# Kernel tuning notes

Measured on AMD Instinct MI355X. Metric: run time of the kernel, lower is better.

Reference implementation:

```python
import jax, jax.numpy as jnp
import numpy as np

B, S, D_MODEL, D_FF, N_EXPERTS, TOP_K = 4, 1024, 1024, 4096, 24, 2


def setup_inputs() -> dict:
    key = jax.random.key(0)
    ks = jax.random.split(key, 7)
    sd = 1.0 / np.sqrt(D_MODEL)
    sf = 1.0 / np.sqrt(D_FF)
    return {
        "x": jax.random.normal(ks[0], (B, S, D_MODEL), jnp.float32),
        "gate_w": jax.random.uniform(ks[1], (D_MODEL, N_EXPERTS), jnp.float32, -sd, sd),
        "gate_b": jax.random.uniform(ks[2], (N_EXPERTS,), jnp.float32, -sd, sd),
        "w1": jax.random.uniform(ks[3], (N_EXPERTS, D_MODEL, D_FF), jnp.float32, -sd, sd),
        "b1": jax.random.uniform(ks[4], (N_EXPERTS, D_FF), jnp.float32, -sd, sd),
        "w2": jax.random.uniform(ks[5], (N_EXPERTS, D_FF, D_MODEL), jnp.float32, -sf, sf),
        "b2": jax.random.uniform(ks[6], (N_EXPERTS, D_MODEL), jnp.float32, -sf, sf),
    }


def reference(x, gate_w, gate_b, w1, b1, w2, b2):
    b, s, d = x.shape
    xt = x.reshape(-1, d)                      # [T, d_model]
    t = xt.shape[0]
    scores = xt @ gate_w + gate_b              # [T, E]
    topv, topi = jax.lax.top_k(scores, TOP_K)  # [T, k]
    gates = jax.nn.softmax(topv, axis=-1)      # softmax over the top-k logits
    # combine weights per (token, expert); zero for unselected experts
    cw = jnp.zeros((t, N_EXPERTS), x.dtype).at[jnp.arange(t)[:, None], topi].add(gates)
    out = jnp.zeros_like(xt)
    for e in range(N_EXPERTS):
        h = jax.nn.gelu(xt @ w1[e] + b1[e], approximate=False)
        y = h @ w2[e] + b2[e]
        out = out + cw[:, e:e + 1] * y
    return out.reshape(b, s, d)
```

## Files before the change

### kernel.cpp

```cpp
#include <hip/hip_runtime.h>
#include <hip/hip_bf16.h>
#include <math.h>

#define T_TOKENS 4096
#define DMODEL 1024
#define DFF 4096
#define NEXP 24
#define NSLOTS 8192
#define BKP 40

typedef __attribute__((ext_vector_type(8))) short bf16x8;
typedef __attribute__((ext_vector_type(4))) float f32x4;
typedef __attribute__((ext_vector_type(8))) unsigned short us8;

static __device__ __forceinline__ unsigned short f2bf(float f) {
    union { float f; unsigned u; } v; v.f = f;
    unsigned r = v.u + 0x7fffu + ((v.u >> 16) & 1u);
    return (unsigned short)(r >> 16);
}

__global__ void k_zero(int* __restrict__ p) { p[threadIdx.x] = 0; }

__global__ __launch_bounds__(256) void k_gate(
    const float* __restrict__ x, const float* __restrict__ gw,
    const float* __restrict__ gb, int* __restrict__ topk_e,
    float* __restrict__ topk_g, int* __restrict__ counts)
{
    __shared__ float xs[8][1024];
    __shared__ float sc[8][24];
    __shared__ int lcnt[24];
    int tid = threadIdx.x;
    int t0 = blockIdx.x * 8;
    #pragma unroll
    for (int i = 0; i < 8; i++) {
        int idx = tid + 256*i;
        int r = idx >> 8, c4 = (idx & 255) * 4;
        *(float4*)&xs[r][c4] = *(const float4*)(x + (size_t)(t0+r)*DMODEL + c4);
    }
    if (tid < 24) lcnt[tid] = 0;
    __syncthreads();

    int tok = tid >> 5, e = tid & 31;
    if (e < NEXP) {
        float s0=0.f, s1=0.f, s2=0.f, s3=0.f;
        #pragma unroll 4
        for (int d = 0; d < DMODEL; d += 4) {
            s0 += xs[tok][d]   * gw[(d  )*NEXP + e];
            s1 += xs[tok][d+1] * gw[(d+1)*NEXP + e];
            s2 += xs[tok][d+2] * gw[(d+2)*NEXP + e];
            s3 += xs[tok][d+3] * gw[(d+3)*NEXP + e];
        }
        sc[tok][e] = (s0+s1)+(s2+s3) + gb[e];
    }
    __syncthreads();

    if (tid < 8) {
        int t = t0 + tid;
        float v0=-1e30f, v1=-1e30f; int i0=0, i1=0;
        #pragma unroll
        for (int ee = 0; ee < NEXP; ee++) {
            float s = sc[tid][ee];
            if (s > v0) { v1=v0; i1=i0; v0=s; i0=ee; }
            else if (s > v1) { v1=s; i1=ee; }
        }
        float e1 = expf(v1 - v0);
        float g0 = 1.f/(1.f+e1), g1 = e1/(1.f+e1);
        topk_e[t*2]=i0; topk_e[t*2+1]=i1;
        topk_g[t*2]=g0; topk_g[t*2+1]=g1;
        atomicAdd(&lcnt[i0], 1); atomicAdd(&lcnt[i1], 1);
    }
    __syncthreads();
    if (tid < NEXP && lcnt[tid]) atomicAdd(&counts[tid], lcnt[tid]);
}

__global__ void k_scan(const int* __restrict__ counts, int* __restrict__ offsets) {
    if (threadIdx.x == 0) {
        int run = 0;
        for (int e = 0; e < NEXP; e++) { offsets[e] = run; run += counts[e]; }
        offsets[NEXP] = run;
    }
}

__global__ __launch_bounds__(256) void k_assign(
    const int* __restrict__ topk_e, const float* __restrict__ topk_g,
    const int* __restrict__ offsets, int* __restrict__ counts2,
    int* __restrict__ slot_token, float* __restrict__ slot_gate,
    int* __restrict__ slot_of)
{
    int idx = blockIdx.x * 256 + threadIdx.x;
    if (idx >= NSLOTS) return;
    int e = topk_e[idx];
    int pos = offsets[e] + atomicAdd(&counts2[e], 1);
    slot_token[pos] = idx >> 1;
    slot_gate[pos] = topk_g[idx];
    slot_of[idx] = pos;
}

__global__ __launch_bounds__(256) void k_xgather(
    const float* __restrict__ x, const int* __restrict__ slot_token,
    unsigned short* __restrict__ xg)
{
    int idx = blockIdx.x * 256 + threadIdx.x;
    int slot = idx >> 7, c8 = (idx & 127) * 8;
    int tok = slot_token[slot];
    const float4* p = (const float4*)(x + (size_t)tok * DMODEL + c8);
    float4 v0 = p[0], v1 = p[1];
    us8 o;
    o[0]=f2bf(v0.x); o[1]=f2bf(v0.y); o[2]=f2bf(v0.z); o[3]=f2bf(v0.w);
    o[4]=f2bf(v1.x); o[5]=f2bf(v1.y); o[6]=f2bf(v1.z); o[7]=f2bf(v1.w);
    *(us8*)(xg + (size_t)slot * DMODEL + c8) = o;
}


#define FFN_BODY(LDA, LDB, NTT)                                                \
    int tid = threadIdx.x, l = tid & 63, wv = tid >> 6;                        \
    int wm = (wv >> 1) * 48, wn = (wv & 1) * 64;                               \
    int lrow = l & 15, lkg = l >> 4;                                           \
    f32x4 acc[3][4];                                                           \
    _Pragma("unroll")                                                          \
    for (int i = 0; i < 3; i++)                                                \
      _Pragma("unroll")                                                        \
      for (int j = 0; j < 4; j++)                                              \
        acc[i][j] = (f32x4){0.f, 0.f, 0.f, 0.f};                               \
    int n4 = (tid & 31) * 4;                                                   \
    int dwk = tid >> 5;                          \
    int arow0 = tid >> 2, ac0 = tid & 3;                                       \
    int arow1 = 128 + (tid >> 2);                                              \
    int apc0 = ac0 ^ ((arow0 >> 1) & 3);                                       \
    int apc1 = ac0 ^ ((arow1 >> 1) & 3);                                       \
    int mBw = (tid & 31) & 7;                  \
    int pdw = 2 * ((dwk >> 1) ^ mBw) + (dwk & 1);                              \
    float4 br0, br1; us8 ar0, ar1;                                             \
    auto issue = [&](int t) {                                                  \
        int k0 = t * 32;                                                       \
        const float* p = wb + (size_t)(k0 + dwk*2) * LDB + n4;                 \
        br0 = *(const float4*)p;                                               \
        br1 = *(const float4*)(p + LDB);                                       \
        ar0 = *(const us8*)(ag + (size_t)arow0 * LDA + k0 + ac0 * 8);          \
        if (tid < 256)                                                         \
            ar1 = *(const us8*)(ag + (size_t)arow1 * LDA + k0 + ac0 * 8);      \
    };                                                                         \
    auto wr = [&]() {                                                          \
        _Pragma("unroll")                                                      \
        for (int j = 0; j < 4; j++) {                                          \
            int nn = n4 + j;                                                   \
            unsigned u;                                                        \
            asm("v_cvt_pk_bf16_f32 %0, %1, %2" : "=v"(u)                       \
                : "v"(((const float*)&br0)[j]), "v"(((const float*)&br1)[j])); \
            *(unsigned*)&Bs[nn*BKP + 2*pdw] = u;                               \
        }                                                                      \
        *(us8*)&As[arow0*32 + apc0*8] = ar0;                                   \
        if (tid < 256)                                                         \
            *(us8*)&As[arow1*32 + apc1*8] = ar1;                               \
    };                                                                         \
    issue(0);                                                                  \
    for (int t = 0; t < NTT; t++) {                                            \
        __syncthreads();                                                       \
        wr();                                                                  \
        if (t + 1 < NTT) issue(t + 1);                                         \
        __syncthreads();                                                       \
        bf16x8 a[3];                                                           \
        _Pragma("unroll")                                                      \
        for (int ms = 0; ms < 3; ms++) {                                       \
            int r = wm + ms*16 + lrow;                                         \
            int c = lkg ^ ((r >> 1) & 3);                                      \
            a[ms] = *(const bf16x8*)&As[r*32 + c*8];                           \
        }                                                                      \
        union BV { uint2 q[2]; bf16x8 v; } b[4];                               \
        _Pragma("unroll")                                                      \
        for (int ni = 0; ni < 4; ni++) {                                       \
            int nb = wn + ni*16 + lrow;                                        \
            int mB = (nb >> 2) & 7;                                            \
            b[ni].q[0] = *(const uint2*)&Bs[nb*BKP + 4*((2*lkg) ^ mB)];        \
            b[ni].q[1] = *(const uint2*)&Bs[nb*BKP + 4*((2*lkg + 1) ^ mB)];    \
        }                                                                      \
        _Pragma("unroll")                                                      \
        for (int ms = 0; ms < 3; ms++)                                         \
          _Pragma("unroll")                                                    \
          for (int ni = 0; ni < 4; ni++)                                       \
            acc[ms][ni] = __builtin_amdgcn_mfma_f32_16x16x32_bf16(             \
                a[ms], b[ni].v, acc[ms][ni], 0, 0, 0);                         \
    }

__global__ __launch_bounds__(512) void k_ffn1(
    const unsigned short* __restrict__ xg, const float* __restrict__ w1,
    const float* __restrict__ b1, const int* __restrict__ offsets,
    unsigned short* __restrict__ hbuf)
{
    int bid = blockIdx.x;
    int xcd = bid & 7, s = bid >> 3;
    int eg = s / 96, rem = s % 96;
    int nx = rem / 3, mt = rem % 3;
    int e = eg * 8 + xcd;

    int base = offsets[e], ne = offsets[e+1] - base;
    if (mt * 192 >= ne) return;
    int n0 = nx * 128;
    int slotbase = base + mt * 192;

    __shared__ unsigned short As[192*32];
    __shared__ unsigned short Bs[128*BKP];

    const unsigned short* ag = xg + (size_t)slotbase * DMODEL;
    const float* wb = w1 + (size_t)e * DMODEL * DFF + n0;

    FFN_BODY(DMODEL, DFF, (DMODEL/32))

    #pragma unroll
    for (int ms = 0; ms < 3; ms++) {
        #pragma unroll
        for (int ni = 0; ni < 4; ni++) {
            int n = n0 + wn + ni*16 + lrow;
            float bias = b1[e*DFF + n];
            #pragma unroll
            for (int r = 0; r < 4; r++) {
                int ml = wm + ms*16 + lkg*4 + r;
                if (mt*192 + ml < ne) {
                    float hv = acc[ms][ni][r] + bias;
                    hv = 0.5f * hv * (1.f + erff(hv * 0.70710678118f));
                    hbuf[(size_t)(slotbase + ml) * DFF + n] = f2bf(hv);
                }
            }
        }
    }
}

__global__ __launch_bounds__(512) void k_ffn2(
    const unsigned short* __restrict__ hbuf, const float* __restrict__ w2,
    const float* __restrict__ b2, const int* __restrict__ offsets,
    const float* __restrict__ slot_gate, float* __restrict__ y)
{
    int bid = blockIdx.x;
    int xcd = bid & 7, s = bid >> 3;
    int eg = s / 24, rem = s % 24;
    int nx = rem / 3, mt = rem % 3;
    int e = eg * 8 + xcd;

    int base = offsets[e], ne = offsets[e+1] - base;
    if (mt * 192 >= ne) return;
    int n0 = nx * 128;
    int slotbase = base + mt * 192;

    __shared__ unsigned short As[192*32];
    __shared__ unsigned short Bs[128*BKP];
    __shared__ float gat[192];

    if (threadIdx.x < 192)
        gat[threadIdx.x] = (mt*192 + threadIdx.x < ne) ? slot_gate[slotbase + threadIdx.x] : 0.f;

    const unsigned short* ag = hbuf + (size_t)slotbase * DFF;
    const float* wb = w2 + (size_t)e * DFF * DMODEL + n0;

    FFN_BODY(DFF, DMODEL, (DFF/32))

    #pragma unroll
    for (int ms = 0; ms < 3; ms++) {
        #pragma unroll
        for (int ni = 0; ni < 4; ni++) {
            int n = n0 + wn + ni*16 + lrow;
            float bias = b2[e*DMODEL + n];
            #pragma unroll
            for (int r = 0; r < 4; r++) {
                int ml = wm + ms*16 + lkg*4 + r;
                if (mt*192 + ml < ne) {
                    y[(size_t)(slotbase + ml) * DMODEL + n] = gat[ml] * (acc[ms][ni][r] + bias);
                }
            }
        }
    }
}

__global__ __launch_bounds__(256) void k_combine(
    const float* __restrict__ y, const int* __restrict__ slot_of,
    float* __restrict__ out)
{
    int t = blockIdx.x, tid = threadIdx.x;
    int s0 = slot_of[t*2], s1 = slot_of[t*2+1];
    float4 a = ((const float4*)(y + (size_t)s0 * DMODEL))[tid];
    float4 b = ((const float4*)(y + (size_t)s1 * DMODEL))[tid];
    float4 o = {a.x+b.x, a.y+b.y, a.z+b.z, a.w+b.w};
    ((float4*)(out + (size_t)t * DMODEL))[tid] = o;
}

extern "C" void kernel_launch(void* const* d_in, const int* in_sizes, int n_in,
                              void* d_out, int out_size, void* d_ws, size_t ws_size,
                              hipStream_t stream) {
    const float* x  = (const float*)d_in[0];
    const float* gw = (const float*)d_in[1];
    const float* gb = (const float*)d_in[2];
    const float* w1 = (const float*)d_in[3];
    const float* b1 = (const float*)d_in[4];
    const float* w2 = (const float*)d_in[5];
    const float* b2 = (const float*)d_in[6];
    float* out = (float*)d_out;
    char* ws = (char*)d_ws;

    int*   counts     = (int*)(ws + 0);
    int*   counts2    = (int*)(ws + 128);
    int*   offsets    = (int*)(ws + 256);
    int*   topk_e     = (int*)(ws + 512);
    float* topk_g     = (float*)(ws + 33280);
    int*   slot_token = (int*)(ws + 66048);
    float* slot_gate  = (float*)(ws + 99328);
    int*   slot_of    = (int*)(ws + 132608);
    unsigned short* xg = (unsigned short*)(ws + 1048576);
    float*          y  = (float*)(ws + 1048576);
    unsigned short* hbuf = (unsigned short*)(ws + 35651584);

    k_zero<<<1, 128, 0, stream>>>((int*)ws);

    k_gate<<<T_TOKENS/8, 256, 0, stream>>>(x, gw, gb, topk_e, topk_g, counts);
    k_scan<<<1, 64, 0, stream>>>(counts, offsets);
    k_assign<<<NSLOTS/256, 256, 0, stream>>>(topk_e, topk_g, offsets, counts2,
                                             slot_token, slot_gate, slot_of);
    k_xgather<<<NSLOTS*128/256, 256, 0, stream>>>(x, slot_token, xg);

    k_ffn1<<<dim3(8 * 288), 512, 0, stream>>>(xg, w1, b1, offsets, hbuf);

    k_ffn2<<<dim3(8 * 72), 512, 0, stream>>>(hbuf, w2, b2, offsets, slot_gate, y);

    k_combine<<<T_TOKENS, 256, 0, stream>>>(y, slot_of, out);
}
```

Measured before the change: 463.0 us.

## Double-buffer A via direct global-to-LDS loads and retile FFN GEMMs to 128x128

Rewrites the shared FFN GEMM body. The A operand is now copied straight from global memory into double-buffered LDS with global_load_lds, and explicit waitcnt/barrier scheduling lets the next tile's loads overlap the current compute. Blocks shrink from 512 threads with 192-row tiles to 256 threads with 128-row tiles, each wave computing 64x64. This aims to hide load latency and cut register staging, but adds launch-grid blocks and relies on hand-written vmcnt counts that must stay exact.

```diff
diff --git a/kernel.cpp b/kernel.cpp
--- a/kernel.cpp
+++ b/kernel.cpp
@@ -17,6 +17,12 @@
     union { float f; unsigned u; } v; v.f = f;
     unsigned r = v.u + 0x7fffu + ((v.u >> 16) & 1u);
     return (unsigned short)(r >> 16);
+}
+
+typedef const __attribute__((address_space(1))) void gvoid_t;
+typedef __attribute__((address_space(3))) void lvoid_t;
+static __device__ __forceinline__ void gl_lds16(const void* g, void* l) {
+    __builtin_amdgcn_global_load_lds((gvoid_t*)g, (lvoid_t*)l, 16, 0, 0);
 }
 
 __global__ void k_zero(int* __restrict__ p) { p[threadIdx.x] = 0; }
@@ -112,102 +118,123 @@
 }
 
 
-#define FFN_BODY(LDA, LDB, NTT)                                                \
+#define FFN_PIPE(LDA, LDB, NTT)                                                \
     int tid = threadIdx.x, l = tid & 63, wv = tid >> 6;                        \
-    int wm = (wv >> 1) * 48, wn = (wv & 1) * 64;                               \
+    int wm = (wv >> 1) * 64, wn = (wv & 1) * 64;                               \
     int lrow = l & 15, lkg = l >> 4;                                           \
-    f32x4 acc[3][4];                                                           \
+    f32x4 acc[4][4];                                                           \
     _Pragma("unroll")                                                          \
-    for (int i = 0; i < 3; i++)                                                \
+    for (int i = 0; i < 4; i++)                                                \
       _Pragma("unroll")                                                        \
       for (int j = 0; j < 4; j++)                                              \
         acc[i][j] = (f32x4){0.f, 0.f, 0.f, 0.f};                               \
-    int n4 = (tid & 31) * 4;                                                   \
-    int dwk = tid >> 5;                          \
-    int arow0 = tid >> 2, ac0 = tid & 3;                                       \
-    int arow1 = 128 + (tid >> 2);                                              \
-    int apc0 = ac0 ^ ((arow0 >> 1) & 3);                                       \
-    int apc1 = ac0 ^ ((arow1 >> 1) & 3);                                       \
-    int mBw = (tid & 31) & 7;                  \
-    int pdw = 2 * ((dwk >> 1) ^ mBw) + (dwk & 1);                              \
-    float4 br0, br1; us8 ar0, ar1;                                             \
-    auto issue = [&](int t) {                                                  \
-        int k0 = t * 32;                                                       \
-        const float* p = wb + (size_t)(k0 + dwk*2) * LDB + n4;                 \
-        br0 = *(const float4*)p;                                               \
-        br1 = *(const float4*)(p + LDB);                                       \
-        ar0 = *(const us8*)(ag + (size_t)arow0 * LDA + k0 + ac0 * 8);          \
-        if (tid < 256)                                                         \
-            ar1 = *(const us8*)(ag + (size_t)arow1 * LDA + k0 + ac0 * 8);      \
+    int n4 = (tid & 31) * 4, q7 = tid & 7, kq = (tid >> 5) * 4;                \
+    int cbw = (tid >> 5) ^ q7;                   \
+    int ar0 = tid >> 2;                                                        \
+    int as0 = (tid & 3) ^ ((ar0 >> 1) & 3);                                    \
+    int ar1 = 64 + ar0;                                                        \
+    int as1 = (tid & 3) ^ ((ar1 >> 1) & 3);                                    \
+    float4 br[4];                                                              \
+    auto issueB = [&](int t) {                                                 \
+        const float* pp = wb + (size_t)(t*32 + kq) * LDB + n4;                 \
+        br[0] = *(const float4*)pp;                                            \
+        br[1] = *(const float4*)(pp + LDB);                                    \
+        br[2] = *(const float4*)(pp + 2*LDB);                                  \
+        br[3] = *(const float4*)(pp + 3*LDB);                                  \
     };                                                                         \
-    auto wr = [&]() {                                                          \
+    auto writeB = [&]() {                                                      \
         _Pragma("unroll")                                                      \
         for (int j = 0; j < 4; j++) {                                          \
-            int nn = n4 + j;                                                   \
-            unsigned u;                                                        \
-            asm("v_cvt_pk_bf16_f32 %0, %1, %2" : "=v"(u)                       \
-                : "v"(((const float*)&br0)[j]), "v"(((const float*)&br1)[j])); \
-            *(unsigned*)&Bs[nn*BKP + 2*pdw] = u;                               \
+            unsigned u01, u23;                                                 \
+            asm("v_cvt_pk_bf16_f32 %0, %1, %2" : "=v"(u01)                     \
+                : "v"(((const float*)&br[0])[j]), "v"(((const float*)&br[1])[j])); \
+            asm("v_cvt_pk_bf16_f32 %0, %1, %2" : "=v"(u23)                     \
+                : "v"(((const float*)&br[2])[j]), "v"(((const float*)&br[3])[j])); \
+            uint2 u; u.x = u01; u.y = u23;                                     \
+            *(uint2*)&Bs[(n4 + j)*BKP + cbw*4] = u;                            \
         }                                                                      \
-        *(us8*)&As[arow0*32 + apc0*8] = ar0;                                   \
-        if (tid < 256)                                                         \
-            *(us8*)&As[arow1*32 + apc1*8] = ar1;                               \
     };                                                                         \
-    issue(0);                                                                  \
-    for (int t = 0; t < NTT; t++) {                                            \
-        __syncthreads();                                                       \
-        wr();                                                                  \
-        if (t + 1 < NTT) issue(t + 1);                                         \
-        __syncthreads();                                                       \
-        bf16x8 a[3];                                                           \
+    auto stageA = [&](int p, int t) {                                          \
+        int k0 = t * 32;                                                       \
+        char* dst = (char*)As[p];                                              \
+        gl_lds16(ag + (size_t)ar0 * LDA + k0 + as0 * 8, dst + tid*16);         \
+        gl_lds16(ag + (size_t)ar1 * LDA + k0 + as1 * 8, dst + 4096 + tid*16);  \
+    };                                                                         \
+    auto compute = [&](int p) {                                                \
+        bf16x8 a[4];                                                           \
         _Pragma("unroll")                                                      \
-        for (int ms = 0; ms < 3; ms++) {                                       \
+        for (int ms = 0; ms < 4; ms++) {                                       \
             int r = wm + ms*16 + lrow;                                         \
             int c = lkg ^ ((r >> 1) & 3);                                      \
-            a[ms] = *(const bf16x8*)&As[r*32 + c*8];                           \
+            a[ms] = *(const bf16x8*)&As[p][r*32 + c*8];                        \
         }                                                                      \
-        union BV { uint2 q[2]; bf16x8 v; } b[4];                               \
+        union BV { uint2 qq[2]; bf16x8 v; } b[4];                              \
         _Pragma("unroll")                                                      \
         for (int ni = 0; ni < 4; ni++) {                                       \
             int nb = wn + ni*16 + lrow;                                        \
-            int mB = (nb >> 2) & 7;                                            \
-            b[ni].q[0] = *(const uint2*)&Bs[nb*BKP + 4*((2*lkg) ^ mB)];        \
-            b[ni].q[1] = *(const uint2*)&Bs[nb*BKP + 4*((2*lkg + 1) ^ mB)];    \
+            int qb = (nb >> 2) & 7;                                            \
+            b[ni].qq[0] = *(const uint2*)&Bs[nb*BKP + ((2*lkg)   ^ qb)*4];     \
+            b[ni].qq[1] = *(const uint2*)&Bs[nb*BKP + ((2*lkg+1) ^ qb)*4];     \
         }                                                                      \
         _Pragma("unroll")                                                      \
-        for (int ms = 0; ms < 3; ms++)                                         \
+        for (int ms = 0; ms < 4; ms++)                                         \
           _Pragma("unroll")                                                    \
           for (int ni = 0; ni < 4; ni++)                                       \
             acc[ms][ni] = __builtin_amdgcn_mfma_f32_16x16x32_bf16(             \
                 a[ms], b[ni].v, acc[ms][ni], 0, 0, 0);                         \
-    }
-
-__global__ __launch_bounds__(512) void k_ffn1(
+    };                                                                         \
+    issueB(0);                                                                 \
+    stageA(0, 0);                                                              \
+    for (int t = 0; t < NTT - 1; t++) {                                        \
+        int p = t & 1;                                                         \
+        writeB();                              \
+        issueB(t + 1);                                                         \
+        stageA(p ^ 1, t + 1);                                                  \
+        __builtin_amdgcn_sched_barrier(0);                                     \
+        asm volatile("s_waitcnt vmcnt(6) lgkmcnt(0)" ::: "memory");            \
+        __builtin_amdgcn_s_barrier();                                          \
+        __builtin_amdgcn_sched_barrier(0);                                     \
+        compute(p);                                                            \
+        asm volatile("s_waitcnt lgkmcnt(0)" ::: "memory");                     \
+        __builtin_amdgcn_s_barrier();                                          \
+        __builtin_amdgcn_sched_barrier(0);                                     \
+    }                                                                          \
+    {                                                                          \
+        int p = (NTT - 1) & 1;                                                 \
+        writeB();                                                              \
+        __builtin_amdgcn_sched_barrier(0);                                     \
+        asm volatile("s_waitcnt vmcnt(0) lgkmcnt(0)" ::: "memory");            \
+        __builtin_amdgcn_s_barrier();                                          \
+        __builtin_amdgcn_sched_barrier(0);                                     \
+        compute(p);                                                            \
+    }
+
+__global__ __launch_bounds__(256) void k_ffn1(
     const unsigned short* __restrict__ xg, const float* __restrict__ w1,
     const float* __restrict__ b1, const int* __restrict__ offsets,
     unsigned short* __restrict__ hbuf)
 {
     int bid = blockIdx.x;
     int xcd = bid & 7, s = bid >> 3;
-    int eg = s / 96, rem = s % 96;
-    int nx = rem / 3, mt = rem % 3;
+    int eg = s >> 7, rem = s & 127;
+    int nx = rem >> 2, mt = rem & 3;
     int e = eg * 8 + xcd;
 
     int base = offsets[e], ne = offsets[e+1] - base;
-    if (mt * 192 >= ne) return;
+    if (mt * 128 >= ne) return;
     int n0 = nx * 128;
-    int slotbase = base + mt * 192;
-
-    __shared__ unsigned short As[192*32];
+    int slotbase = base + mt * 128;
+
+    __shared__ unsigned short As[2][128*32];
     __shared__ unsigned short Bs[128*BKP];
 
     const unsigned short* ag = xg + (size_t)slotbase * DMODEL;
     const float* wb = w1 + (size_t)e * DMODEL * DFF + n0;
 
-    FFN_BODY(DMODEL, DFF, (DMODEL/32))
+    FFN_PIPE(DMODEL, DFF, (DMODEL/32))
 
     #pragma unroll
-    for (int ms = 0; ms < 3; ms++) {
+    for (int ms = 0; ms < 4; ms++) {
         #pragma unroll
         for (int ni = 0; ni < 4; ni++) {
             int n = n0 + wn + ni*16 + lrow;
@@ -215,7 +242,7 @@
             #pragma unroll
             for (int r = 0; r < 4; r++) {
                 int ml = wm + ms*16 + lkg*4 + r;
-                if (mt*192 + ml < ne) {
+                if (mt*128 + ml < ne) {
                     float hv = acc[ms][ni][r] + bias;
                     hv = 0.5f * hv * (1.f + erff(hv * 0.70710678118f));
                     hbuf[(size_t)(slotbase + ml) * DFF + n] = f2bf(hv);
@@ -225,36 +252,36 @@
     }
 }
 
-__global__ __launch_bounds__(512) void k_ffn2(
+__global__ __launch_bounds__(256) void k_ffn2(
     const unsigned short* __restrict__ hbuf, const float* __restrict__ w2,
     const float* __restrict__ b2, const int* __restrict__ offsets,
     const float* __restrict__ slot_gate, float* __restrict__ y)
 {
     int bid = blockIdx.x;
     int xcd = bid & 7, s = bid >> 3;
-    int eg = s / 24, rem = s % 24;
-    int nx = rem / 3, mt = rem % 3;
+    int eg = s >> 5, rem = s & 31;
+    int nx = rem >> 2, mt = rem & 3;
     int e = eg * 8 + xcd;
 
     int base = offsets[e], ne = offsets[e+1] - base;
-    if (mt * 192 >= ne) return;
+    if (mt * 128 >= ne) return;
     int n0 = nx * 128;
-    int slotbase = base + mt * 192;
-
-    __shared__ unsigned short As[192*32];
+    int slotbase = base + mt * 128;
+
+    __shared__ unsigned short As[2][128*32];
     __shared__ unsigned short Bs[128*BKP];
-    __shared__ float gat[192];
-
-    if (threadIdx.x < 192)
-        gat[threadIdx.x] = (mt*192 + threadIdx.x < ne) ? slot_gate[slotbase + threadIdx.x] : 0.f;
+    __shared__ float gat[128];
+
+    if (threadIdx.x < 128)
+        gat[threadIdx.x] = (mt*128 + threadIdx.x < ne) ? slot_gate[slotbase + threadIdx.x] : 0.f;
 
     const unsigned short* ag = hbuf + (size_t)slotbase * DFF;
     const float* wb = w2 + (size_t)e * DFF * DMODEL + n0;
 
-    FFN_BODY(DFF, DMODEL, (DFF/32))
+    FFN_PIPE(DFF, DMODEL, (DFF/32))
 
     #pragma unroll
-    for (int ms = 0; ms < 3; ms++) {
+    for (int ms = 0; ms < 4; ms++) {
         #pragma unroll
         for (int ni = 0; ni < 4; ni++) {
             int n = n0 + wn + ni*16 + lrow;
@@ -262,7 +289,7 @@
             #pragma unroll
             for (int r = 0; r < 4; r++) {
                 int ml = wm + ms*16 + lkg*4 + r;
-                if (mt*192 + ml < ne) {
+                if (mt*128 + ml < ne) {
                     y[(size_t)(slotbase + ml) * DMODEL + n] = gat[ml] * (acc[ms][ni][r] + bias);
                 }
             }
@@ -315,9 +342,9 @@
                                              slot_token, slot_gate, slot_of);
     k_xgather<<<NSLOTS*128/256, 256, 0, stream>>>(x, slot_token, xg);
 
-    k_ffn1<<<dim3(8 * 288), 512, 0, stream>>>(xg, w1, b1, offsets, hbuf);
-
-    k_ffn2<<<dim3(8 * 72), 512, 0, stream>>>(hbuf, w2, b2, offsets, slot_gate, y);
+    k_ffn1<<<dim3(8 * 384), 256, 0, stream>>>(xg, w1, b1, offsets, hbuf);
+
+    k_ffn2<<<dim3(8 * 96), 256, 0, stream>>>(hbuf, w2, b2, offsets, slot_gate, y);
 
     k_combine<<<T_TOKENS, 256, 0, stream>>>(y, slot_of, out);
 }
```

Measured after the change: 537.3 us. 16.1% more time.
